# Optimization experiments

Hardware: AMD Instinct MI355X
Metric: run time of the kernel (lower is better)

The kernel has to match this reference:

```python
import jax, jax.numpy as jnp
import numpy as np

TOTAL = 131072   # total frames across all utterances
SEG = 256        # number of utterances
FEAT = 78        # input feature dim (hardcoded by Linear(78,1024))
HID = 1024
NCLS = 10


def _linear_params(key, fan_in, fan_out):
    # torch nn.Linear default init: U(-1/sqrt(fan_in), 1/sqrt(fan_in))
    bound = 1.0 / np.sqrt(fan_in)
    kw, kb = jax.random.split(key)
    W = jax.random.uniform(kw, (fan_in, fan_out), minval=-bound, maxval=bound, dtype=jnp.float32)
    b = jax.random.uniform(kb, (fan_out,), minval=-bound, maxval=bound, dtype=jnp.float32)
    return W, b


def setup_inputs() -> dict:
    key = jax.random.key(0)
    ks = jax.random.split(key, 8)
    # ragged lengths summing exactly to TOTAL
    rng = np.random.default_rng(0)
    raw = rng.integers(256, 768, size=SEG).astype(np.float64)
    lens = np.maximum(1, (raw * TOTAL / raw.sum()).astype(np.int64))
    lens[-1] += TOTAL - lens.sum()
    lengths = jnp.asarray(lens, dtype=jnp.int32)

    x = jax.random.normal(ks[0], (TOTAL, FEAT), dtype=jnp.float32)
    W1, b1 = _linear_params(ks[1], FEAT, HID)
    W2, b2 = _linear_params(ks[2], HID, HID)
    W3, b3 = _linear_params(ks[3], HID, HID)
    W4, b4 = _linear_params(ks[4], HID, HID)
    W5, b5 = _linear_params(ks[5], HID, 1)
    W6, b6 = _linear_params(ks[6], HID, HID)
    W7, b7 = _linear_params(ks[7], HID, NCLS)
    return dict(x=x, W1=W1, b1=b1, W2=W2, b2=b2, W3=W3, b3=b3, W4=W4, b4=b4,
                W5=W5, b5=b5, W6=W6, b6=b6, W7=W7, b7=b7, lengths=lengths)


def reference(x, W1, b1, W2, b2, W3, b3, W4, b4, W5, b5, W6, b6, W7, b7, lengths):
    h = jax.nn.relu(x @ W1 + b1)
    h = jax.nn.relu(h @ W2 + b2)
    h = jax.nn.relu(h @ W3 + b3)
    h = jax.nn.relu(h @ W4 + b4)            # [N, HID]
    scores = jax.nn.relu(h @ W5 + b5)[:, 0]  # per-frame attention logit [N]

    # per-segment softmax over frames, then weighted sum pooling (fused segment ops)
    n_seg = lengths.shape[0]
    seg = jnp.repeat(jnp.arange(n_seg, dtype=jnp.int32), lengths,
                     total_repeat_length=h.shape[0])          # [N] segment ids
    m = jax.ops.segment_max(scores, seg, num_segments=n_seg)  # stable softmax max
    e = jnp.exp(scores - m[seg])
    denom = jax.ops.segment_sum(e, seg, num_segments=n_seg)
    w = e / denom[seg]                                        # [N] softmax weights
    pooled = jax.ops.segment_sum(h * w[:, None], seg, num_segments=n_seg)  # [SEG, HID]

    out = jax.nn.relu(pooled @ W6 + b6) @ W7 + b7             # [SEG, 10]
    return out
```

## Files before the change

kernel.cpp:

```cpp
#include <hip/hip_runtime.h>
#include <hip/hip_fp16.h>

#define TOTAL 131072
#define SEGN  256
#define FEAT  78
#define FPAD  96
#define HID   1024
#define NCLS  10
#define FCHUNK 32

typedef __attribute__((ext_vector_type(8))) short short8;
typedef __attribute__((ext_vector_type(4))) float floatx4;

typedef __attribute__((address_space(1))) void gvoid_t;
typedef __attribute__((address_space(3))) void svoid_t;

__device__ __forceinline__ void async_copy16(const void* gsrc, void* ldst) {
    __builtin_amdgcn_global_load_lds((gvoid_t*)(void*)gsrc, (svoid_t*)ldst, 16, 0, 0);
}


__global__ void conv_x_slab(const float* __restrict__ x, __half* __restrict__ xb,
                            int row0, int rows) {
    int idx = blockIdx.x * 256 + threadIdx.x;
    if (idx >= rows * FPAD) return;
    int col = idx % FPAD;
    int r   = idx / FPAD;
    float v = (col < FEAT) ? x[(size_t)(row0 + r) * FEAT + col] : 0.0f;
    xb[idx] = __float2half(v);
}

__global__ void conv_wt_kernel(const float* __restrict__ W, __half* __restrict__ Wt,
                               int K, int N, int Kpad) {
    int idx = blockIdx.x * 256 + threadIdx.x;
    if (idx >= N * Kpad) return;
    int k = idx % Kpad;
    int n = idx / Kpad;
    float v = (k < K) ? W[(size_t)k * N + n] : 0.0f;
    Wt[idx] = __float2half(v);
}

__global__ void conv_w4_kernel(const float* __restrict__ W2, const float* __restrict__ W3,
                               const float* __restrict__ W4, const float* __restrict__ W6,
                               __half* __restrict__ w2t, __half* __restrict__ w3t,
                               __half* __restrict__ w4t, __half* __restrict__ w6t) {
    int idx = blockIdx.x * 256 + threadIdx.x;
    if (idx >= HID * HID) return;
    int k = idx % HID;
    int n = idx / HID;
    const float* Ws[4] = {W2, W3, W4, W6};
    __half* Ts[4] = {w2t, w3t, w4t, w6t};
    int w = blockIdx.y;
    Ts[w][idx] = __float2half(Ws[w][(size_t)k * HID + n]);
}


__global__ __launch_bounds__(256, 2)
void gemm_f16(const __half* __restrict__ A, const __half* __restrict__ Bt,
              __half* __restrict__ C, const float* __restrict__ bias,
              int M, int N, int K, int relu_flag)
{
    __shared__ __align__(16) short smem[4 * 128 * 32];
    short* lds_a0 = smem;
    short* lds_a1 = smem + 128 * 32;
    short* lds_b0 = smem + 2 * 128 * 32;
    short* lds_b1 = smem + 3 * 128 * 32;

    const int t   = threadIdx.x;
    const int nbn = N >> 7;
    const int nbm = M >> 7;
    int bm, bn;
    {
        const int b = blockIdx.x;
        if ((nbm & 7) == 0) {
            const int xcd = b & 7;
            const int j   = b >> 3;
            bm = xcd * (nbm >> 3) + j / nbn;
            bn = j % nbn;
        } else {
            bn = b % nbn;
            bm = b / nbn;
        }
    }
    const size_t m0 = (size_t)bm * 128;
    const size_t n0 = (size_t)bn * 128;
    const int wave = t >> 6, lane = t & 63;
    const int wm = (wave >> 1) << 6;
    const int wn = (wave & 1) << 6;
    const int l16 = lane & 15, q = lane >> 4;

    floatx4 acc[4][4] = {};

    const int c0 = t, c1 = t + 256;
    const __half* a0 = A  + (m0 + (size_t)(c0 >> 2)) * K + (c0 & 3) * 8;
    const __half* a1 = A  + (m0 + (size_t)(c1 >> 2)) * K + (c1 & 3) * 8;
    const __half* b0 = Bt + (n0 + (size_t)(c0 >> 2)) * K + (c0 & 3) * 8;
    const __half* b1 = Bt + (n0 + (size_t)(c1 >> 2)) * K + (c1 & 3) * 8;
    short* lA0_0 = &lds_a0[c0 * 8];
    short* lA0_1 = &lds_a0[c1 * 8];
    short* lA1_0 = &lds_a1[c0 * 8];
    short* lA1_1 = &lds_a1[c1 * 8];
    short* lB0_0 = &lds_b0[c0 * 8];
    short* lB0_1 = &lds_b0[c1 * 8];
    short* lB1_0 = &lds_b1[c0 * 8];
    short* lB1_1 = &lds_b1[c1 * 8];

    for (int k0 = 0; k0 < K; k0 += 64) {
        __syncthreads();
        async_copy16(a0 + k0, lA0_0);
        async_copy16(a1 + k0, lA0_1);
        async_copy16(b0 + k0, lB0_0);
        async_copy16(b1 + k0, lB0_1);
        async_copy16(a0 + k0 + 32, lA1_0);
        async_copy16(a1 + k0 + 32, lA1_1);
        async_copy16(b0 + k0 + 32, lB1_0);
        async_copy16(b1 + k0 + 32, lB1_1);
        __syncthreads();

        short8 af[4], bf[4];
#pragma unroll
        for (int i = 0; i < 4; ++i)
            af[i] = *(const short8*)&lds_a0[(wm + i * 16 + l16) * 32 + q * 8];
#pragma unroll
        for (int i = 0; i < 4; ++i)
            bf[i] = *(const short8*)&lds_b0[(wn + i * 16 + l16) * 32 + q * 8];
#pragma unroll
        for (int mi = 0; mi < 4; ++mi)
#pragma unroll
            for (int ni = 0; ni < 4; ++ni)
                acc[mi][ni] = __builtin_amdgcn_mfma_f32_16x16x32_f16(
                    af[mi], bf[ni], acc[mi][ni], 0, 0, 0);

#pragma unroll
        for (int i = 0; i < 4; ++i)
            af[i] = *(const short8*)&lds_a1[(wm + i * 16 + l16) * 32 + q * 8];
#pragma unroll
        for (int i = 0; i < 4; ++i)
            bf[i] = *(const short8*)&lds_b1[(wn + i * 16 + l16) * 32 + q * 8];
#pragma unroll
        for (int mi = 0; mi < 4; ++mi)
#pragma unroll
            for (int ni = 0; ni < 4; ++ni)
                acc[mi][ni] = __builtin_amdgcn_mfma_f32_16x16x32_f16(
                    af[mi], bf[ni], acc[mi][ni], 0, 0, 0);
    }

    __half* ct = (__half*)smem;
#pragma unroll
    for (int h = 0; h < 2; ++h) {
        __syncthreads();
        if (wm == h * 64) {
#pragma unroll
            for (int ni = 0; ni < 4; ++ni) {
                const int col = wn + ni * 16 + l16;
                const float bv = bias[n0 + col];
#pragma unroll
                for (int mi = 0; mi < 4; ++mi) {
                    const int r0l = mi * 16 + q * 4;
#pragma unroll
                    for (int r = 0; r < 4; ++r) {
                        float v = acc[mi][ni][r] + bv;
                        if (relu_flag) v = fmaxf(v, 0.0f);
                        ct[(r0l + r) * 128 + col] = __float2half(v);
                    }
                }
            }
        }
        __syncthreads();
#pragma unroll
        for (int it = 0; it < 4; ++it) {
            const int chunk = it * 256 + t;
            const int row = chunk >> 4;
            const int off = (chunk & 15) * 8;
            *(short8*)&C[(m0 + h * 64 + row) * N + n0 + off] =
                *(const short8*)&ct[row * 128 + off];
        }
    }
}


__global__ __launch_bounds__(256, 2)
void gemm_k96(const __half* __restrict__ A, const __half* __restrict__ Bt,
              __half* __restrict__ C, const float* __restrict__ bias, int M, int N)
{
    __shared__ __align__(16) short smem[2 * 128 * 96];
    short* lds_a = smem;
    short* lds_b = smem + 128 * 96;

    const int t   = threadIdx.x;
    const int nbn = N >> 7;
    const int nbm = M >> 7;
    int bm, bn;
    {
        const int b = blockIdx.x;
        if ((nbm & 7) == 0) {
            const int xcd = b & 7;
            const int j   = b >> 3;
            bm = xcd * (nbm >> 3) + j / nbn;
            bn = j % nbn;
        } else {
            bn = b % nbn;
            bm = b / nbn;
        }
    }
    const size_t m0 = (size_t)bm * 128;
    const size_t n0 = (size_t)bn * 128;
    const int wave = t >> 6, lane = t & 63;
    const int wm = (wave >> 1) << 6;
    const int wn = (wave & 1) << 6;
    const int l16 = lane & 15, q = lane >> 4;

#pragma unroll
    for (int i = 0; i < 6; ++i) {
        const int c = i * 256 + t;
        const int r = c / 12, j = c % 12;
        async_copy16(A  + (m0 + (size_t)r) * 96 + j * 8, &lds_a[c * 8]);
        async_copy16(Bt + (n0 + (size_t)r) * 96 + j * 8, &lds_b[c * 8]);
    }
    __syncthreads();

    floatx4 acc[4][4] = {};
#pragma unroll
    for (int ks = 0; ks < 3; ++ks) {
        short8 af[4], bf[4];
        const int xo = ks * 32 + q * 8;
#pragma unroll
        for (int i = 0; i < 4; ++i)
            af[i] = *(const short8*)&lds_a[(wm + i * 16 + l16) * 96 + xo];
#pragma unroll
        for (int i = 0; i < 4; ++i)
            bf[i] = *(const short8*)&lds_b[(wn + i * 16 + l16) * 96 + xo];
#pragma unroll
        for (int mi = 0; mi < 4; ++mi)
#pragma unroll
            for (int ni = 0; ni < 4; ++ni)
                acc[mi][ni] = __builtin_amdgcn_mfma_f32_16x16x32_f16(
                    af[mi], bf[ni], acc[mi][ni], 0, 0, 0);
    }

    __half* ct = (__half*)smem;
#pragma unroll
    for (int h = 0; h < 2; ++h) {
        __syncthreads();
        if (wm == h * 64) {
#pragma unroll
            for (int ni = 0; ni < 4; ++ni) {
                const int col = wn + ni * 16 + l16;
                const float bv = bias[n0 + col];
#pragma unroll
                for (int mi = 0; mi < 4; ++mi) {
                    const int r0l = mi * 16 + q * 4;
#pragma unroll
                    for (int r = 0; r < 4; ++r) {
                        float v = fmaxf(acc[mi][ni][r] + bv, 0.0f);
                        ct[(r0l + r) * 128 + col] = __float2half(v);
                    }
                }
            }
        }
        __syncthreads();
#pragma unroll
        for (int it = 0; it < 4; ++it) {
            const int chunk = it * 256 + t;
            const int row = chunk >> 4;
            const int off = (chunk & 15) * 8;
            *(short8*)&C[(m0 + h * 64 + row) * N + n0 + off] =
                *(const short8*)&ct[row * 128 + off];
        }
    }
}


__global__ void seg_offsets_kernel(const int* __restrict__ lengths, int* __restrict__ off) {
    if (blockIdx.x == 0 && threadIdx.x == 0) {
        int a = 0;
        off[0] = 0;
        for (int i = 0; i < SEGN; ++i) { a += lengths[i]; off[i + 1] = a; }
    }
}


__global__ __launch_bounds__(256)
void scorepool_kernel(const __half* __restrict__ h4, int slab_beg,
                      const float* __restrict__ W5, const float* __restrict__ b5,
                      const int* __restrict__ segoff,
                      float* __restrict__ pooled, float* __restrict__ denom)
{
    __shared__ float e_sh[FCHUNK];
    const int t = threadIdx.x, wave = t >> 6, lane = t & 63;
    const int f0 = slab_beg + blockIdx.x * FCHUNK;
    const float b5v = b5[0];

#pragma unroll
    for (int i = 0; i < 8; ++i) {
        const int fl = wave * 8 + i;
        const __half* row = h4 + (size_t)(f0 - slab_beg + fl) * HID + lane * 16;
        const float* wv = W5 + lane * 16;
        short8 r0 = *(const short8*)row;
        short8 r1 = *(const short8*)(row + 8);
        float s = 0.f;
#pragma unroll
        for (int j = 0; j < 8; ++j) s += __half2float(((const __half*)&r0)[j]) * wv[j];
#pragma unroll
        for (int j = 0; j < 8; ++j) s += __half2float(((const __half*)&r1)[j]) * wv[j + 8];
#pragma unroll
        for (int o = 32; o > 0; o >>= 1) s += __shfl_down(s, o);
        if (lane == 0)
            e_sh[fl] = __expf(fminf(fmaxf(s + b5v, 0.0f), 80.0f));
    }
    __syncthreads();

    const int c0 = t * 4;
    int lo = 0, hi = SEGN - 1;
    while (lo < hi) {
        int mid = (lo + hi + 1) >> 1;
        if (segoff[mid] <= f0) lo = mid; else hi = mid - 1;
    }
    int s = lo;
    int f = f0;
    const int fend = f0 + FCHUNK;
    const __half* base = h4 + (size_t)(f0 - slab_beg) * HID + c0;
    while (f < fend) {
        int send = segoff[s + 1];
        if (send > fend) send = fend;
        float a0 = 0.f, a1 = 0.f, a2 = 0.f, a3 = 0.f, es = 0.f;
        for (; f < send; ++f, base += HID) {
            float e = e_sh[f - f0];
            const __half2* r2 = (const __half2*)base;
            float2 u = __half22float2(r2[0]);
            float2 v = __half22float2(r2[1]);
            a0 += e * u.x; a1 += e * u.y; a2 += e * v.x; a3 += e * v.y;
            es += e;
        }
        float* p = pooled + (size_t)s * HID + c0;
        atomicAdd(p,     a0);
        atomicAdd(p + 1, a1);
        atomicAdd(p + 2, a2);
        atomicAdd(p + 3, a3);
        if (t == 0) atomicAdd(&denom[s], es);
        ++s;
    }
}


__global__ __launch_bounds__(256)
void finalize_pool_kernel(const float* __restrict__ pooled, const float* __restrict__ denom,
                          __half* __restrict__ poolh)
{
    int s = blockIdx.x, t = threadIdx.x;
    float inv = 1.0f / denom[s];
    for (int j = t; j < HID; j += 256)
        poolh[(size_t)s * HID + j] = __float2half(pooled[(size_t)s * HID + j] * inv);
}


__global__ void final_kernel(const __half* __restrict__ z, const float* __restrict__ W7,
                             const float* __restrict__ b7, float* __restrict__ out) {
    int s = blockIdx.x, t = threadIdx.x;
    float loc[NCLS];
#pragma unroll
    for (int c = 0; c < NCLS; ++c) loc[c] = 0.f;
    for (int k = t; k < HID; k += 256) {
        float zk = __half2float(z[(size_t)s * HID + k]);
        const float* wr = W7 + k * NCLS;
#pragma unroll
        for (int c = 0; c < NCLS; ++c) loc[c] += zk * wr[c];
    }
#pragma unroll
    for (int c = 0; c < NCLS; ++c)
#pragma unroll
        for (int o = 32; o > 0; o >>= 1) loc[c] += __shfl_down(loc[c], o);
    __shared__ float accs[NCLS];
    if (t < NCLS) accs[t] = 0.f;
    __syncthreads();
    if ((t & 63) == 0)
        for (int c = 0; c < NCLS; ++c) atomicAdd(&accs[c], loc[c]);
    __syncthreads();
    if (t < NCLS) out[s * NCLS + t] = accs[t] + b7[t];
}


extern "C" void kernel_launch(void* const* d_in, const int* in_sizes, int n_in,
                              void* d_out, int out_size, void* d_ws, size_t ws_size,
                              hipStream_t stream) {
    const float* x  = (const float*)d_in[0];
    const float* W1 = (const float*)d_in[1];
    const float* b1 = (const float*)d_in[2];
    const float* W2 = (const float*)d_in[3];
    const float* b2 = (const float*)d_in[4];
    const float* W3 = (const float*)d_in[5];
    const float* b3 = (const float*)d_in[6];
    const float* W4 = (const float*)d_in[7];
    const float* b4 = (const float*)d_in[8];
    const float* W5 = (const float*)d_in[9];
    const float* b5 = (const float*)d_in[10];
    const float* W6 = (const float*)d_in[11];
    const float* b6 = (const float*)d_in[12];
    const float* W7 = (const float*)d_in[13];
    const float* b7 = (const float*)d_in[14];
    const int* lengths = (const int*)d_in[15];
    float* out = (float*)d_out;

    char* ws = (char*)d_ws;
    size_t off = 0;
    auto take = [&](size_t bytes) -> char* {
        char* p = ws + off;
        off = (off + bytes + 255) & ~(size_t)255;
        return p;
    };
    __half* w1t   = (__half*)take((size_t)HID * FPAD * 2);
    __half* w2t   = (__half*)take((size_t)HID * HID * 2);
    __half* w3t   = (__half*)take((size_t)HID * HID * 2);
    __half* w4t   = (__half*)take((size_t)HID * HID * 2);
    __half* w6t   = (__half*)take((size_t)HID * HID * 2);
    int*    segoff = (int*)take((SEGN + 1) * 4);
    float*  pooled = (float*)take((size_t)SEGN * HID * 4);
    float*  denom  = (float*)take(SEGN * 4);
    __half* poolh  = (__half*)take((size_t)SEGN * HID * 2);
    __half* z      = (__half*)take((size_t)SEGN * HID * 2);

    int R = TOTAL;
    while (R > 1024) {
        size_t need = off + (size_t)R * FPAD * 2 + 2 * (size_t)R * HID * 2 + 3 * 256;
        if (need <= ws_size) break;
        R >>= 1;
    }
    __half* slabX = (__half*)take((size_t)R * FPAD * 2);
    __half* slabA = (__half*)take((size_t)R * HID * 2);
    __half* slabB = (__half*)take((size_t)R * HID * 2);

    seg_offsets_kernel<<<1, 64, 0, stream>>>(lengths, segoff);
    hipMemsetAsync(pooled, 0, (size_t)SEGN * HID * 4, stream);
    hipMemsetAsync(denom, 0, SEGN * 4, stream);

    conv_wt_kernel<<<(HID * FPAD + 255) / 256, 256, 0, stream>>>(W1, w1t, FEAT, HID, FPAD);
    dim3 gW((HID * HID + 255) / 256, 4);
    conv_w4_kernel<<<gW, 256, 0, stream>>>(W2, W3, W4, W6, w2t, w3t, w4t, w6t);

    const int nBlocksSlab = (R / 128) * (HID / 128);
    for (int sb = 0; sb < TOTAL; sb += R) {
        conv_x_slab<<<(R * FPAD + 255) / 256, 256, 0, stream>>>(x, slabX, sb, R);
        gemm_k96<<<nBlocksSlab, 256, 0, stream>>>(slabX, w1t, slabA, b1, R, HID);
        gemm_f16<<<nBlocksSlab, 256, 0, stream>>>(slabA, w2t, slabB, b2, R, HID, HID, 1);
        gemm_f16<<<nBlocksSlab, 256, 0, stream>>>(slabB, w3t, slabA, b3, R, HID, HID, 1);
        gemm_f16<<<nBlocksSlab, 256, 0, stream>>>(slabA, w4t, slabB, b4, R, HID, HID, 1);
        scorepool_kernel<<<R / FCHUNK, 256, 0, stream>>>(slabB, sb, W5, b5, segoff, pooled, denom);
    }

    finalize_pool_kernel<<<SEGN, 256, 0, stream>>>(pooled, denom, poolh);
    const int nBlocksHead = (SEGN / 128) * (HID / 128);
    gemm_f16<<<nBlocksHead, 256, 0, stream>>>(poolh, w6t, z, b6, SEGN, HID, HID, 1);
    final_kernel<<<SEGN, 256, 0, stream>>>(z, W7, b7, out);
}
```

Baseline: 1.330 ms.

## Load B fragments directly from global into registers, halve LDS in GEMMs

Both f16 GEMM kernels stop staging the B (weight) tile through LDS. Each wave now loads its MFMA B fragments straight from global memory into registers, and only A goes through async copies into LDS. This halves shared memory per block, and launch bounds are raised from 2 to 3 blocks per CU to use the freed space. The cost is uncoalesced 16-byte global loads for B, duplicated across the two waves that share each column slice, plus added register pressure that may cause spills at the higher occupancy target.

```diff
diff --git a/kernel.cpp b/kernel.cpp
--- a/kernel.cpp
+++ b/kernel.cpp
@@ -55,16 +55,14 @@
 }
 
 
-__global__ __launch_bounds__(256, 2)
+__global__ __launch_bounds__(256, 3)
 void gemm_f16(const __half* __restrict__ A, const __half* __restrict__ Bt,
               __half* __restrict__ C, const float* __restrict__ bias,
               int M, int N, int K, int relu_flag)
 {
-    __shared__ __align__(16) short smem[4 * 128 * 32];
+    __shared__ __align__(16) short smem[2 * 128 * 32];
     short* lds_a0 = smem;
     short* lds_a1 = smem + 128 * 32;
-    short* lds_b0 = smem + 2 * 128 * 32;
-    short* lds_b1 = smem + 3 * 128 * 32;
 
     const int t   = threadIdx.x;
     const int nbn = N >> 7;
@@ -92,57 +90,53 @@
     floatx4 acc[4][4] = {};
 
     const int c0 = t, c1 = t + 256;
-    const __half* a0 = A  + (m0 + (size_t)(c0 >> 2)) * K + (c0 & 3) * 8;
-    const __half* a1 = A  + (m0 + (size_t)(c1 >> 2)) * K + (c1 & 3) * 8;
-    const __half* b0 = Bt + (n0 + (size_t)(c0 >> 2)) * K + (c0 & 3) * 8;
-    const __half* b1 = Bt + (n0 + (size_t)(c1 >> 2)) * K + (c1 & 3) * 8;
+    const __half* a0 = A + (m0 + (size_t)(c0 >> 2)) * K + (c0 & 3) * 8;
+    const __half* a1 = A + (m0 + (size_t)(c1 >> 2)) * K + (c1 & 3) * 8;
     short* lA0_0 = &lds_a0[c0 * 8];
     short* lA0_1 = &lds_a0[c1 * 8];
     short* lA1_0 = &lds_a1[c0 * 8];
     short* lA1_1 = &lds_a1[c1 * 8];
-    short* lB0_0 = &lds_b0[c0 * 8];
-    short* lB0_1 = &lds_b0[c1 * 8];
-    short* lB1_0 = &lds_b1[c0 * 8];
-    short* lB1_1 = &lds_b1[c1 * 8];
+
+    const __half* bp[4];
+#pragma unroll
+    for (int i = 0; i < 4; ++i)
+        bp[i] = Bt + (n0 + (size_t)(wn + i * 16 + l16)) * K + q * 8;
 
     for (int k0 = 0; k0 < K; k0 += 64) {
         __syncthreads();
         async_copy16(a0 + k0, lA0_0);
         async_copy16(a1 + k0, lA0_1);
-        async_copy16(b0 + k0, lB0_0);
-        async_copy16(b1 + k0, lB0_1);
         async_copy16(a0 + k0 + 32, lA1_0);
         async_copy16(a1 + k0 + 32, lA1_1);
-        async_copy16(b0 + k0 + 32, lB1_0);
-        async_copy16(b1 + k0 + 32, lB1_1);
-        __syncthreads();
-
-        short8 af[4], bf[4];
+
+        short8 bf0[4], bf1[4];
+#pragma unroll
+        for (int i = 0; i < 4; ++i) bf0[i] = *(const short8*)(bp[i] + k0);
+#pragma unroll
+        for (int i = 0; i < 4; ++i) bf1[i] = *(const short8*)(bp[i] + k0 + 32);
+
+        __syncthreads();
+
+        short8 af[4];
 #pragma unroll
         for (int i = 0; i < 4; ++i)
             af[i] = *(const short8*)&lds_a0[(wm + i * 16 + l16) * 32 + q * 8];
 #pragma unroll
-        for (int i = 0; i < 4; ++i)
-            bf[i] = *(const short8*)&lds_b0[(wn + i * 16 + l16) * 32 + q * 8];
-#pragma unroll
         for (int mi = 0; mi < 4; ++mi)
 #pragma unroll
             for (int ni = 0; ni < 4; ++ni)
                 acc[mi][ni] = __builtin_amdgcn_mfma_f32_16x16x32_f16(
-                    af[mi], bf[ni], acc[mi][ni], 0, 0, 0);
+                    af[mi], bf0[ni], acc[mi][ni], 0, 0, 0);
 
 #pragma unroll
         for (int i = 0; i < 4; ++i)
             af[i] = *(const short8*)&lds_a1[(wm + i * 16 + l16) * 32 + q * 8];
 #pragma unroll
-        for (int i = 0; i < 4; ++i)
-            bf[i] = *(const short8*)&lds_b1[(wn + i * 16 + l16) * 32 + q * 8];
-#pragma unroll
         for (int mi = 0; mi < 4; ++mi)
 #pragma unroll
             for (int ni = 0; ni < 4; ++ni)
                 acc[mi][ni] = __builtin_amdgcn_mfma_f32_16x16x32_f16(
-                    af[mi], bf[ni], acc[mi][ni], 0, 0, 0);
+                    af[mi], bf1[ni], acc[mi][ni], 0, 0, 0);
     }
 
     __half* ct = (__half*)smem;
@@ -179,13 +173,12 @@
 }
 
 
-__global__ __launch_bounds__(256, 2)
+__global__ __launch_bounds__(256, 3)
 void gemm_k96(const __half* __restrict__ A, const __half* __restrict__ Bt,
               __half* __restrict__ C, const float* __restrict__ bias, int M, int N)
 {
-    __shared__ __align__(16) short smem[2 * 128 * 96];
+    __shared__ __align__(16) short smem[128 * 96];
     short* lds_a = smem;
-    short* lds_b = smem + 128 * 96;
 
     const int t   = threadIdx.x;
     const int nbn = N >> 7;
@@ -214,28 +207,33 @@
     for (int i = 0; i < 6; ++i) {
         const int c = i * 256 + t;
         const int r = c / 12, j = c % 12;
-        async_copy16(A  + (m0 + (size_t)r) * 96 + j * 8, &lds_a[c * 8]);
-        async_copy16(Bt + (n0 + (size_t)r) * 96 + j * 8, &lds_b[c * 8]);
+        async_copy16(A + (m0 + (size_t)r) * 96 + j * 8, &lds_a[c * 8]);
+    }
+
+    short8 bf[4][3];
+#pragma unroll
+    for (int i = 0; i < 4; ++i) {
+        const __half* bp = Bt + (n0 + (size_t)(wn + i * 16 + l16)) * 96 + q * 8;
+#pragma unroll
+        for (int ks = 0; ks < 3; ++ks)
+            bf[i][ks] = *(const short8*)(bp + ks * 32);
     }
     __syncthreads();
 
     floatx4 acc[4][4] = {};
 #pragma unroll
     for (int ks = 0; ks < 3; ++ks) {
-        short8 af[4], bf[4];
+        short8 af[4];
         const int xo = ks * 32 + q * 8;
 #pragma unroll
         for (int i = 0; i < 4; ++i)
             af[i] = *(const short8*)&lds_a[(wm + i * 16 + l16) * 96 + xo];
 #pragma unroll
-        for (int i = 0; i < 4; ++i)
-            bf[i] = *(const short8*)&lds_b[(wn + i * 16 + l16) * 96 + xo];
-#pragma unroll
         for (int mi = 0; mi < 4; ++mi)
 #pragma unroll
             for (int ni = 0; ni < 4; ++ni)
                 acc[mi][ni] = __builtin_amdgcn_mfma_f32_16x16x32_f16(
-                    af[mi], bf[ni], acc[mi][ni], 0, 0, 0);
+                    af[mi], bf[ni][ks], acc[mi][ni], 0, 0, 0);
     }
 
     __half* ct = (__half*)smem;
```

Result: slower. 2.135 ms (+60.5%).
